# Kernel optimization log

Measured on AMD Instinct MI355X. Metric: run time of the kernel, lower is better.

The kernel has to match this reference:

```python
import jax, jax.numpy as jnp
import numpy as np

DIM = 768
NUM_HEADS = 12
HEAD_DIM = DIM // NUM_HEADS
HW = 32  # input_size = (32, 32)


def setup_inputs() -> dict:
    key = jax.random.key(0)
    ks = jax.random.split(key, 7)
    return {
        "x": jax.random.normal(ks[0], (8, HW, HW, DIM), dtype=jnp.float32),
        "w_qkv": jax.random.normal(ks[1], (DIM, 3 * DIM), dtype=jnp.float32) * 0.02,
        "b_qkv": jnp.zeros((3 * DIM,), dtype=jnp.float32),
        "w_proj": jax.random.normal(ks[2], (DIM, DIM), dtype=jnp.float32) * 0.02,
        "b_proj": jnp.zeros((DIM,), dtype=jnp.float32),
        "rel_pos_h": jax.random.normal(ks[3], (2 * HW - 1, HEAD_DIM), dtype=jnp.float32) * 0.02,
        "rel_pos_w": jax.random.normal(ks[4], (2 * HW - 1, HEAD_DIM), dtype=jnp.float32) * 0.02,
    }


def _gather_rel_pos(size, rel_pos):
    # q_size == k_size == size, so no resize; index = i - j + (size - 1)
    idx = jnp.arange(size)[:, None] - jnp.arange(size)[None, :] + (size - 1)
    return rel_pos[idx]  # [size, size, head_dim]


def reference(x, w_qkv, b_qkv, w_proj, b_proj, rel_pos_h, rel_pos_w):
    B, H, W, C = x.shape
    nH, D = NUM_HEADS, HEAD_DIM
    scale = D ** -0.5
    S = H * W

    qkv = x.reshape(B, S, C) @ w_qkv + b_qkv          # [B,S,3C]
    qkv = qkv.reshape(B, S, 3, nH, D).transpose(2, 0, 3, 1, 4)  # [3,B,nH,S,D]
    q, k, v = qkv[0], qkv[1], qkv[2]

    attn = jnp.einsum('bnsd,bntd->bnst', q * scale, k)  # [B,nH,S,S]

    # decomposed relative positional bias
    Rh = _gather_rel_pos(H, rel_pos_h)                  # [H,H,D]
    Rw = _gather_rel_pos(W, rel_pos_w)                  # [W,W,D]
    r_q = q.reshape(B, nH, H, W, D)
    rel_h = jnp.einsum('bnhwc,hkc->bnhwk', r_q, Rh)     # [B,nH,H,W,H]
    rel_w = jnp.einsum('bnhwc,wkc->bnhwk', r_q, Rw)     # [B,nH,H,W,W]
    attn = (attn.reshape(B, nH, H, W, H, W)
            + rel_h[..., :, None]
            + rel_w[..., None, :]).reshape(B, nH, S, S)

    attn = jax.nn.softmax(attn, axis=-1)
    out = jnp.einsum('bnst,bntd->bnsd', attn, v)        # [B,nH,S,D]
    out = out.transpose(0, 2, 1, 3).reshape(B, H, W, C)
    return out @ w_proj + b_proj
```

## Files before the change

### kernel.cpp

```cpp
#include <hip/hip_runtime.h>
#include <cstdint>
#include <cstddef>

#define NH 12
#define HDIM 64
#define C_ 768
#define C3 2304
#define SEQ 1024
#define LS 72
#define LSV 76
#define SMAX 6.0f
#define LOG2E 1.4426950408889634f

typedef short bf16x8_t __attribute__((ext_vector_type(8)));
typedef float f32x4_t __attribute__((ext_vector_type(4)));
typedef unsigned short u16x4_t __attribute__((ext_vector_type(4)));

__device__ __forceinline__ unsigned short bf16_rne(float x) {
    unsigned int u = __float_as_uint(x);
    u += 0x7FFFu + ((u >> 16) & 1u);
    return (unsigned short)(u >> 16);
}
__device__ __forceinline__ float bf16f(unsigned short h) {
    return __uint_as_float(((unsigned int)h) << 16);
}

__device__ __forceinline__ void load_lds16(const unsigned short* g, unsigned short* l) {
    auto gp = (const __attribute__((address_space(1))) unsigned short*)(uintptr_t)g;
    auto lp = (__attribute__((address_space(3))) unsigned short*)(uint32_t)(uintptr_t)l;
    __builtin_amdgcn_global_load_lds(gp, lp, 16, 0, 0);
}

__device__ __forceinline__ int swz(int row, int g) {
    const int pr = row >> 1;
    const int ch = (((row & 1) << 2) | g) ^ (pr & 7);
    return pr * 64 + ch * 8;
}

__device__ __forceinline__ void splitT_body(const float* __restrict__ W,
                                            unsigned short* __restrict__ Thi,
                                            unsigned short* __restrict__ Tlo,
                                            int Kdim, int Ndim, int kb, int nb,
                                            float (*tile)[33], int t)
{
    const int lr = t >> 3, lc = (t & 7) * 4;
    *(float4*)&tile[lr][lc] = *(const float4*)&W[(size_t)(kb + lr) * Ndim + nb + lc];
    __syncthreads();
    const float v0 = tile[lc + 0][lr];
    const float v1 = tile[lc + 1][lr];
    const float v2 = tile[lc + 2][lr];
    const float v3 = tile[lc + 3][lr];
    u16x4_t h, l;
    h.x = bf16_rne(v0); l.x = bf16_rne(v0 - bf16f(h.x));
    h.y = bf16_rne(v1); l.y = bf16_rne(v1 - bf16f(h.y));
    h.z = bf16_rne(v2); l.z = bf16_rne(v2 - bf16f(h.z));
    h.w = bf16_rne(v3); l.w = bf16_rne(v3 - bf16f(h.w));
    *(u16x4_t*)&Thi[(size_t)(nb + lr) * Kdim + kb + lc] = h;
    *(u16x4_t*)&Tlo[(size_t)(nb + lr) * Kdim + kb + lc] = l;
}

__global__ __launch_bounds__(256)
void prep_kernel(const float* __restrict__ x, const float* __restrict__ w_qkv,
                 const float* __restrict__ w_proj,
                 const float* __restrict__ rel_h, const float* __restrict__ rel_w,
                 unsigned short* __restrict__ xhi,
                 unsigned short* __restrict__ wqh, unsigned short* __restrict__ wql,
                 unsigned short* __restrict__ wph, unsigned short* __restrict__ wpl,
                 unsigned short* __restrict__ relcat)
{
    __shared__ float tile[32][33];
    const int bid = blockIdx.x, tid = threadIdx.x;
    if (bid < 6144) {
        const int i = bid * 256 + tid;
        float4 v = ((const float4*)x)[i];
        u16x4_t h;
        h.x = bf16_rne(v.x); h.y = bf16_rne(v.y); h.z = bf16_rne(v.z); h.w = bf16_rne(v.w);
        ((u16x4_t*)xhi)[i] = h;
    } else if (bid < 7872) {
        const int local = bid - 6144;
        const int bx = local % 72, by = local / 72;
        splitT_body(w_qkv, wqh, wql, C_, C3, by * 32, bx * 32, tile, tid);
    } else if (bid < 8448) {
        const int local = bid - 7872;
        const int bx = local % 24, by = local / 24;
        splitT_body(w_proj, wph, wpl, C_, C_, by * 32, bx * 32, tile, tid);
    } else {
        const int i = (bid - 8448) * 256 + tid;
        if (i < 2016) {
            const int j = i * 4;
            const int row = j >> 6, col = j & 63;
            const float* src = row < 63 ? &rel_h[row * 64 + col] : &rel_w[(row - 63) * 64 + col];
            const float4 v = *(const float4*)src;
            u16x4_t h;
            h.x = bf16_rne(v.x); h.y = bf16_rne(v.y); h.z = bf16_rne(v.z); h.w = bf16_rne(v.w);
            *(u16x4_t*)&relcat[j] = h;
        }
    }
}

__global__ __launch_bounds__(256, 4)
void qkvgemm_kernel(const unsigned short* __restrict__ Ahi, const unsigned short* __restrict__ BThi,
                    const float* __restrict__ bias,
                    unsigned short* __restrict__ q_hi, unsigned short* __restrict__ k_hi,
                    unsigned short* __restrict__ v_hi)
{
    constexpr int K = 768;
    __shared__ unsigned short As[2][4096];
    __shared__ unsigned short Bs[2][4096];
    const int tid = threadIdx.x;
    const int w = tid >> 6, lane = tid & 63, g = lane >> 4, r = lane & 15;
    const int wr = (w >> 1) * 64, wc = (w & 1) * 64;

    const int bid  = blockIdx.x;
    const int xcd  = bid & 7;
    const int idx  = bid >> 3;
    const int msub = idx & 7;
    const int ntile = idx >> 3;
    const int m0 = (xcd * 8 + msub) * 128;
    const int n0 = ntile * 128;

    int row_[2], gc_[2];
#pragma unroll
    for (int i = 0; i < 2; ++i) {
        const int s = i * 256 + tid;
        const int pr = s >> 3;
        const int u = (s & 7) ^ (pr & 7);
        row_[i] = pr * 2 + (u >> 2);
        gc_[i]  = u & 3;
    }
    const unsigned short* gA0 = Ahi + (size_t)(m0 + row_[0]) * K + gc_[0] * 8;
    const unsigned short* gA1 = Ahi + (size_t)(m0 + row_[1]) * K + gc_[1] * 8;
    const unsigned short* gB0 = BThi + (size_t)(n0 + row_[0]) * K + gc_[0] * 8;
    const unsigned short* gB1 = BThi + (size_t)(n0 + row_[1]) * K + gc_[1] * 8;
    const int lofs0 = w * 512;
    const int lofs1 = 2048 + w * 512;

    f32x4_t acc[4][4];
#pragma unroll
    for (int i = 0; i < 4; ++i)
#pragma unroll
        for (int j = 0; j < 4; ++j)
#pragma unroll
            for (int q = 0; q < 4; ++q) acc[i][j][q] = 0.f;

    load_lds16(gA0, &As[0][lofs0]);
    load_lds16(gA1, &As[0][lofs1]);
    load_lds16(gB0, &Bs[0][lofs0]);
    load_lds16(gB1, &Bs[0][lofs1]);

    int cur = 0;
    for (int k0 = 0; k0 < K; k0 += 32) {
        __syncthreads();
        if (k0 + 32 < K) {
            const int nb2 = cur ^ 1;
            load_lds16(gA0 + k0 + 32, &As[nb2][lofs0]);
            load_lds16(gA1 + k0 + 32, &As[nb2][lofs1]);
            load_lds16(gB0 + k0 + 32, &Bs[nb2][lofs0]);
            load_lds16(gB1 + k0 + 32, &Bs[nb2][lofs1]);
        }
        bf16x8_t am[4];
#pragma unroll
        for (int i = 0; i < 4; ++i)
            am[i] = *(const bf16x8_t*)&As[cur][swz(wr + 16 * i + r, g)];
        __builtin_amdgcn_s_setprio(1);
#pragma unroll
        for (int j = 0; j < 4; ++j) {
            const bf16x8_t bn = *(const bf16x8_t*)&Bs[cur][swz(wc + 16 * j + r, g)];
#pragma unroll
            for (int i = 0; i < 4; ++i)
                acc[i][j] = __builtin_amdgcn_mfma_f32_16x16x32_bf16(am[i], bn, acc[i][j], 0, 0, 0);
        }
        __builtin_amdgcn_s_setprio(0);
        cur ^= 1;
    }

    const int third = n0 >= 1536 ? 2 : (n0 >= 768 ? 1 : 0);
    unsigned short* outH = third == 2 ? v_hi : third == 1 ? k_hi : q_hi;
#pragma unroll
    for (int j = 0; j < 4; ++j) {
        const int n = n0 + wc + 16 * j + r;
        const float bj = bias[n];
        const int nn = n - third * 768;
        const int h = nn >> 6, d = nn & 63;
#pragma unroll
        for (int i = 0; i < 4; ++i) {
            const int m = m0 + wr + 16 * i + 4 * g;
            const int b = m >> 10, t = m & 1023;
            const size_t hb = ((size_t)(b * NH + h)) << 16;
            unsigned short* dh = outH + hb + (size_t)t * 64 + d;
#pragma unroll
            for (int q = 0; q < 4; ++q)
                dh[(size_t)q * 64] = bf16_rne(acc[i][j][q] + bj);
        }
    }
}

__global__ __launch_bounds__(256, 2)
void projgemm_kernel(const unsigned short* __restrict__ Ahi, const unsigned short* __restrict__ Alo,
                     const unsigned short* __restrict__ BThi, const unsigned short* __restrict__ BTlo,
                     const float* __restrict__ bias, float* __restrict__ C)
{
    constexpr int K = 768;
    constexpr int N = C_;
    __shared__ unsigned short Ash[2][4096], Asl[2][4096];
    __shared__ unsigned short Bsh[2][4096], Bsl[2][4096];
    const int tid = threadIdx.x;
    const int w = tid >> 6, lane = tid & 63, g = lane >> 4, r = lane & 15;
    const int wr = (w >> 1) * 64, wc = (w & 1) * 64;

    const int bid  = blockIdx.x;
    const int xcd  = bid & 7;
    const int idx  = bid >> 3;
    const int msub = idx & 7;
    const int ntile = idx >> 3;
    const int m0 = (xcd * 8 + msub) * 128;
    const int n0 = ntile * 128;

    int row_[2], gc_[2];
#pragma unroll
    for (int i = 0; i < 2; ++i) {
        const int s = i * 256 + tid;
        const int pr = s >> 3;
        const int u = (s & 7) ^ (pr & 7);
        row_[i] = pr * 2 + (u >> 2);
        gc_[i]  = u & 3;
    }
    const unsigned short* gAh0 = Ahi + (size_t)(m0 + row_[0]) * K + gc_[0] * 8;
    const unsigned short* gAh1 = Ahi + (size_t)(m0 + row_[1]) * K + gc_[1] * 8;
    const unsigned short* gAl0 = Alo + (size_t)(m0 + row_[0]) * K + gc_[0] * 8;
    const unsigned short* gAl1 = Alo + (size_t)(m0 + row_[1]) * K + gc_[1] * 8;
    const unsigned short* gBh0 = BThi + (size_t)(n0 + row_[0]) * K + gc_[0] * 8;
    const unsigned short* gBh1 = BThi + (size_t)(n0 + row_[1]) * K + gc_[1] * 8;
    const unsigned short* gBl0 = BTlo + (size_t)(n0 + row_[0]) * K + gc_[0] * 8;
    const unsigned short* gBl1 = BTlo + (size_t)(n0 + row_[1]) * K + gc_[1] * 8;
    const int lofs0 = w * 512;
    const int lofs1 = 2048 + w * 512;

    f32x4_t acc[4][4];
#pragma unroll
    for (int i = 0; i < 4; ++i)
#pragma unroll
        for (int j = 0; j < 4; ++j)
#pragma unroll
            for (int q = 0; q < 4; ++q) acc[i][j][q] = 0.f;

    load_lds16(gAh0, &Ash[0][lofs0]);
    load_lds16(gAh1, &Ash[0][lofs1]);
    load_lds16(gAl0, &Asl[0][lofs0]);
    load_lds16(gAl1, &Asl[0][lofs1]);
    load_lds16(gBh0, &Bsh[0][lofs0]);
    load_lds16(gBh1, &Bsh[0][lofs1]);
    load_lds16(gBl0, &Bsl[0][lofs0]);
    load_lds16(gBl1, &Bsl[0][lofs1]);

    int cur = 0;
    for (int k0 = 0; k0 < K; k0 += 32) {
        __syncthreads();
        if (k0 + 32 < K) {
            const int nb2 = cur ^ 1;
            load_lds16(gAh0 + k0 + 32, &Ash[nb2][lofs0]);
            load_lds16(gAh1 + k0 + 32, &Ash[nb2][lofs1]);
            load_lds16(gAl0 + k0 + 32, &Asl[nb2][lofs0]);
            load_lds16(gAl1 + k0 + 32, &Asl[nb2][lofs1]);
            load_lds16(gBh0 + k0 + 32, &Bsh[nb2][lofs0]);
            load_lds16(gBh1 + k0 + 32, &Bsh[nb2][lofs1]);
            load_lds16(gBl0 + k0 + 32, &Bsl[nb2][lofs0]);
            load_lds16(gBl1 + k0 + 32, &Bsl[nb2][lofs1]);
        }
        bf16x8_t amh[4], aml[4];
#pragma unroll
        for (int i = 0; i < 4; ++i) {
            const int o = swz(wr + 16 * i + r, g);
            amh[i] = *(const bf16x8_t*)&Ash[cur][o];
            aml[i] = *(const bf16x8_t*)&Asl[cur][o];
        }
        __builtin_amdgcn_s_setprio(1);
#pragma unroll
        for (int j = 0; j < 4; ++j) {
            const int o = swz(wc + 16 * j + r, g);
            const bf16x8_t bnh = *(const bf16x8_t*)&Bsh[cur][o];
            const bf16x8_t bnl = *(const bf16x8_t*)&Bsl[cur][o];
#pragma unroll
            for (int i = 0; i < 4; ++i) {
                acc[i][j] = __builtin_amdgcn_mfma_f32_16x16x32_bf16(amh[i], bnh, acc[i][j], 0, 0, 0);
                acc[i][j] = __builtin_amdgcn_mfma_f32_16x16x32_bf16(amh[i], bnl, acc[i][j], 0, 0, 0);
                acc[i][j] = __builtin_amdgcn_mfma_f32_16x16x32_bf16(aml[i], bnh, acc[i][j], 0, 0, 0);
            }
        }
        __builtin_amdgcn_s_setprio(0);
        cur ^= 1;
    }

#pragma unroll
    for (int j = 0; j < 4; ++j) {
        const float bj = bias[n0 + wc + 16 * j + r];
#pragma unroll
        for (int i = 0; i < 4; ++i) {
            float* Cp = C + (size_t)(m0 + wr + 16 * i + 4 * g) * N + n0 + wc + 16 * j + r;
#pragma unroll
            for (int q = 0; q < 4; ++q)
                Cp[(size_t)q * N] = acc[i][j][q] + bj;
        }
    }
}

__global__ __launch_bounds__(256, 4)
void relgemm_kernel(const unsigned short* __restrict__ qhi, const unsigned short* __restrict__ relcat,
                    unsigned short* __restrict__ G)
{
    __shared__ unsigned short bs[128 * LS];
    const int tid = threadIdx.x;
    const int sb = blockIdx.x, bh = blockIdx.y;
    const int w = tid >> 6, lane = tid & 63, g = lane >> 4, r = lane & 15;
    const size_t hb = (size_t)bh << 16;

    {
        const int row = tid >> 1, c32 = (tid & 1) * 32;
        if (row < 126) {
#pragma unroll
            for (int e = 0; e < 4; ++e)
                *(bf16x8_t*)&bs[row * LS + c32 + 8 * e] =
                    *(const bf16x8_t*)&relcat[row * 64 + c32 + 8 * e];
        } else {
            const bf16x8_t z = {0,0,0,0,0,0,0,0};
#pragma unroll
            for (int e = 0; e < 4; ++e)
                *(bf16x8_t*)&bs[row * LS + c32 + 8 * e] = z;
        }
    }
    bf16x8_t aq[2][2];
#pragma unroll
    for (int i = 0; i < 2; ++i)
#pragma unroll
        for (int c = 0; c < 2; ++c)
            aq[i][c] = *(const bf16x8_t*)(qhi + hb + (size_t)(sb * 128 + w * 32 + 16 * i + r) * 64 + c * 32 + 8 * g);
    __syncthreads();

    f32x4_t acc[2][8];
#pragma unroll
    for (int i = 0; i < 2; ++i)
#pragma unroll
        for (int fj = 0; fj < 8; ++fj)
#pragma unroll
            for (int q = 0; q < 4; ++q) acc[i][fj][q] = 0.f;

#pragma unroll
    for (int c = 0; c < 2; ++c)
#pragma unroll
        for (int fj = 0; fj < 8; ++fj) {
            const bf16x8_t brel = *(const bf16x8_t*)&bs[(16 * fj + r) * LS + c * 32 + 8 * g];
#pragma unroll
            for (int i = 0; i < 2; ++i)
                acc[i][fj] = __builtin_amdgcn_mfma_f32_16x16x32_bf16(aq[i][c], brel, acc[i][fj], 0, 0, 0);
        }

    unsigned short* Gb = G + (((size_t)bh << 10) + sb * 128 + w * 32) * 128;
#pragma unroll
    for (int i = 0; i < 2; ++i)
#pragma unroll
        for (int reg = 0; reg < 4; ++reg) {
            unsigned short* Gr = Gb + (size_t)(16 * i + 4 * g + reg) * 128 + r;
#pragma unroll
            for (int fj = 0; fj < 8; ++fj)
                Gr[16 * fj] = bf16_rne(acc[i][fj][reg]);
        }
}

__global__ __launch_bounds__(256, 4)
void attn11_kernel(const unsigned short* __restrict__ qhi,
                   const unsigned short* __restrict__ khi,
                   const unsigned short* __restrict__ vhi,
                   const unsigned short* __restrict__ G,
                   unsigned short* __restrict__ outh, unsigned short* __restrict__ outl)
{
    __shared__ unsigned short ksh[2 * 64 * LS];
    __shared__ unsigned short vsh[2 * 64 * LSV];

    const int tid  = threadIdx.x;
    const int bh   = blockIdx.x;
    const int s0   = blockIdx.y * 64;
    const int w    = tid >> 6;
    const int lane = tid & 63;
    const int g    = lane >> 4;
    const int r    = lane & 15;
    const size_t hb = (size_t)bh << 16;

    bf16x8_t aq[2];
#pragma unroll
    for (int c = 0; c < 2; ++c)
        aq[c] = *(const bf16x8_t*)(qhi + hb + (size_t)(s0 + w * 16 + r) * 64 + c * 32 + 8 * g);

    const unsigned short* Gbh = G + ((size_t)bh << 17);
    const int q    = s0 + w * 16 + r;
    const int qoff = q * 128;
    const int qcb  = (q >> 5) + 31;
    const int iw   = q & 31;
    float bw[4][2];
#pragma unroll
    for (int reg = 0; reg < 4; ++reg)
#pragma unroll
        for (int jh = 0; jh < 2; ++jh)
            bw[reg][jh] = bf16f(Gbh[qoff + 94 + iw - 16 * jh - 4 * g - reg]) * LOG2E;

    f32x4_t oacc[4];
    float lsum[4];
#pragma unroll
    for (int i = 0; i < 4; ++i) {
        lsum[i] = 0.f;
#pragma unroll
        for (int j = 0; j < 4; ++j) oacc[i][j] = 0.f;
    }

    const int krow = tid >> 2, kc16 = (tid & 3) * 16;
    const int tb = (tid >> 4) * 4, d0 = (tid & 15) * 4;
    const int addr_a = (((g & 1) << 5) + r) << 2;
    const int addr_b = addr_a + 64;
    const bool lowg = g < 2;

    {
        const unsigned short* kh = khi + hb + (size_t)krow * 64 + kc16;
        const bf16x8_t a0 = *(const bf16x8_t*)kh;
        const bf16x8_t a1 = *(const bf16x8_t*)(kh + 8);
        u16x4_t rv[4];
#pragma unroll
        for (int i = 0; i < 4; ++i)
            rv[i] = *(const u16x4_t*)(vhi + hb + (size_t)(tb + i) * 64 + d0);
        *(bf16x8_t*)&ksh[krow * LS + kc16]     = a0;
        *(bf16x8_t*)&ksh[krow * LS + kc16 + 8] = a1;
#pragma unroll
        for (int c2 = 0; c2 < 4; ++c2) {
            u16x4_t th;
            th.x = rv[0][c2]; th.y = rv[1][c2]; th.z = rv[2][c2]; th.w = rv[3][c2];
            *(u16x4_t*)&vsh[(d0 + c2) * LSV + tb] = th;
        }
    }
    __syncthreads();

    int cur = 0;
    for (int t0 = 0; t0 < SEQ; t0 += 64) {
        const int cok = cur * 64 * LS;
        const int cov = cur * 64 * LSV;
        const int tn = (t0 + 64 < SEQ) ? t0 + 64 : t0;
        bf16x8_t nk0, nk1;
        u16x4_t nv[4];
        {
            const unsigned short* kh = khi + hb + (size_t)(tn + krow) * 64 + kc16;
            nk0 = *(const bf16x8_t*)kh;
            nk1 = *(const bf16x8_t*)(kh + 8);
#pragma unroll
            for (int i = 0; i < 4; ++i)
                nv[i] = *(const u16x4_t*)(vhi + hb + (size_t)(tn + tb + i) * 64 + d0);
        }

        f32x4_t sacc[4];
#pragma unroll
        for (int fj = 0; fj < 4; ++fj)
#pragma unroll
            for (int j = 0; j < 4; ++j) sacc[fj][j] = 0.f;
        __builtin_amdgcn_s_setprio(1);
#pragma unroll
        for (int c = 0; c < 2; ++c)
#pragma unroll
            for (int fj = 0; fj < 4; ++fj) {
                const bf16x8_t bkh = *(const bf16x8_t*)&ksh[cok + (16 * fj + r) * LS + c * 32 + 8 * g];
                sacc[fj] = __builtin_amdgcn_mfma_f32_16x16x32_bf16(bkh, aq[c], sacc[fj], 0, 0, 0);
            }
        __builtin_amdgcn_s_setprio(0);

        const int kh0 = t0 >> 5;
        const float bh0 = (bf16f(Gbh[qoff + qcb - kh0])     - SMAX) * LOG2E;
        const float bh1 = (bf16f(Gbh[qoff + qcb - kh0 - 1]) - SMAX) * LOG2E;
#pragma unroll
        for (int fj = 0; fj < 4; ++fj)
#pragma unroll
            for (int reg = 0; reg < 4; ++reg) {
                const float s = fmaf(sacc[fj][reg], 0.125f * LOG2E,
                                     ((fj >> 1) ? bh1 : bh0) + bw[reg][fj & 1]);
                const float e = exp2f(s);
                sacc[fj][reg] = e;
                lsum[reg] += e;
            }

        unsigned int pk01[4], pk23[4];
#pragma unroll
        for (int fj = 0; fj < 4; ++fj) {
            asm("v_cvt_pk_bf16_f32 %0, %1, %2" : "=v"(pk01[fj]) : "v"(sacc[fj][0]), "v"(sacc[fj][1]));
            asm("v_cvt_pk_bf16_f32 %0, %1, %2" : "=v"(pk23[fj]) : "v"(sacc[fj][2]), "v"(sacc[fj][3]));
        }

#pragma unroll
        for (int c = 0; c < 2; ++c) {
            const int a01A = __builtin_amdgcn_ds_bpermute(addr_a, (int)pk01[2 * c]);
            const int a23A = __builtin_amdgcn_ds_bpermute(addr_a, (int)pk23[2 * c]);
            const int b01A = __builtin_amdgcn_ds_bpermute(addr_b, (int)pk01[2 * c]);
            const int b23A = __builtin_amdgcn_ds_bpermute(addr_b, (int)pk23[2 * c]);
            const int a01B = __builtin_amdgcn_ds_bpermute(addr_a, (int)pk01[2 * c + 1]);
            const int a23B = __builtin_amdgcn_ds_bpermute(addr_a, (int)pk23[2 * c + 1]);
            const int b01B = __builtin_amdgcn_ds_bpermute(addr_b, (int)pk01[2 * c + 1]);
            const int b23B = __builtin_amdgcn_ds_bpermute(addr_b, (int)pk23[2 * c + 1]);
            union { int u[4]; bf16x8_t v; } pf;
            pf.u[0] = lowg ? a01A : a01B;
            pf.u[1] = lowg ? a23A : a23B;
            pf.u[2] = lowg ? b01A : b01B;
            pf.u[3] = lowg ? b23A : b23B;
            __builtin_amdgcn_s_setprio(1);
#pragma unroll
            for (int fd = 0; fd < 4; ++fd) {
                const bf16x8_t bvh = *(const bf16x8_t*)&vsh[cov + (16 * fd + r) * LSV + c * 32 + 8 * g];
                oacc[fd] = __builtin_amdgcn_mfma_f32_16x16x32_bf16(bvh, pf.v, oacc[fd], 0, 0, 0);
            }
            __builtin_amdgcn_s_setprio(0);
        }

        const int nok = (cur ^ 1) * 64 * LS;
        const int nov = (cur ^ 1) * 64 * LSV;
        *(bf16x8_t*)&ksh[nok + krow * LS + kc16]     = nk0;
        *(bf16x8_t*)&ksh[nok + krow * LS + kc16 + 8] = nk1;
#pragma unroll
        for (int c2 = 0; c2 < 4; ++c2) {
            u16x4_t th;
            th.x = nv[0][c2]; th.y = nv[1][c2]; th.z = nv[2][c2]; th.w = nv[3][c2];
            *(u16x4_t*)&vsh[nov + (d0 + c2) * LSV + tb] = th;
        }
        __syncthreads();
        cur ^= 1;
    }

    const int b = bh / NH, h = bh - (bh / NH) * NH;
    float rs = (lsum[0] + lsum[1]) + (lsum[2] + lsum[3]);
    rs += __shfl_xor(rs, 16);
    rs += __shfl_xor(rs, 32);
    const float rinv = 1.f / rs;
    unsigned short* oph = outh + ((size_t)b * SEQ + q) * C_ + h * HDIM + 4 * g;
    unsigned short* opl = outl + ((size_t)b * SEQ + q) * C_ + h * HDIM + 4 * g;
#pragma unroll
    for (int fd = 0; fd < 4; ++fd) {
        u16x4_t hv, lv;
#pragma unroll
        for (int reg = 0; reg < 4; ++reg) {
            const float v = oacc[fd][reg] * rinv;
            const unsigned short hh = bf16_rne(v);
            hv[reg] = hh;
            lv[reg] = bf16_rne(v - bf16f(hh));
        }
        *(u16x4_t*)(oph + 16 * fd) = hv;
        *(u16x4_t*)(opl + 16 * fd) = lv;
    }
}

extern "C" void kernel_launch(void* const* d_in, const int* in_sizes, int n_in,
                              void* d_out, int out_size, void* d_ws, size_t ws_size,
                              hipStream_t stream) {
    (void)in_sizes; (void)n_in; (void)out_size; (void)ws_size;
    const float* x      = (const float*)d_in[0];
    const float* w_qkv  = (const float*)d_in[1];
    const float* b_qkv  = (const float*)d_in[2];
    const float* w_proj = (const float*)d_in[3];
    const float* b_proj = (const float*)d_in[4];
    const float* rel_h  = (const float*)d_in[5];
    const float* rel_w  = (const float*)d_in[6];
    float* out = (float*)d_out;

    char* base = (char*)d_ws;
    unsigned short* xhi    = (unsigned short*)(base + 0);
    unsigned short* xlo    = (unsigned short*)(base + 12582912);
    unsigned short* wqh    = (unsigned short*)(base + 25165824);
    unsigned short* wql    = (unsigned short*)(base + 28704768);
    unsigned short* wph    = (unsigned short*)(base + 32243712);
    unsigned short* wpl    = (unsigned short*)(base + 33423360);
    unsigned short* qhi    = (unsigned short*)(base + 34603008);
    unsigned short* relcat = (unsigned short*)(base + 47185920);
    unsigned short* khi    = (unsigned short*)(base + 59768832);
    unsigned short* vhi    = (unsigned short*)(base + 84934656);
    unsigned short* G      = (unsigned short*)(base + 110100480);
    unsigned short* ohif   = xhi;
    unsigned short* olo    = xlo;

    prep_kernel<<<8456, 256, 0, stream>>>(x, w_qkv, w_proj, rel_h, rel_w,
                                          xhi, wqh, wql, wph, wpl, relcat);
    qkvgemm_kernel<<<1152, 256, 0, stream>>>(xhi, wqh, b_qkv, qhi, khi, vhi);
    {
        dim3 grid(8, 96);
        relgemm_kernel<<<grid, 256, 0, stream>>>(qhi, relcat, G);
    }
    {
        dim3 grid(96, SEQ / 64);
        attn11_kernel<<<grid, 256, 0, stream>>>(qhi, khi, vhi, G, ohif, olo);
    }
    projgemm_kernel<<<384, 256, 0, stream>>>(ohif, olo, wph, wpl, b_proj, out);
}
```

Baseline: 166.8 us.

## Store V transposed from QKV GEMM epilogue and load it directly in attention

The QKV GEMM epilogue now writes V in a per-head [d][t] transposed layout, using 4-wide vector stores along t. The attention kernel can then copy V tiles into shared memory with two 16-byte loads and stores per thread, instead of gathering 4-element pieces and transposing them in registers. The change also drops the s_setprio hints around the MFMA loops in attention. This removes transpose work and narrow global loads from the attention inner loop, at the cost of a differently shaped store pattern in the GEMM epilogue.

```diff
diff --git a/kernel.cpp b/kernel.cpp
--- a/kernel.cpp
+++ b/kernel.cpp
@@ -102,7 +102,7 @@
 void qkvgemm_kernel(const unsigned short* __restrict__ Ahi, const unsigned short* __restrict__ BThi,
                     const float* __restrict__ bias,
                     unsigned short* __restrict__ q_hi, unsigned short* __restrict__ k_hi,
-                    unsigned short* __restrict__ v_hi)
+                    unsigned short* __restrict__ vT)
 {
     constexpr int K = 768;
     __shared__ unsigned short As[2][4096];
@@ -175,22 +175,43 @@
     }
 
     const int third = n0 >= 1536 ? 2 : (n0 >= 768 ? 1 : 0);
-    unsigned short* outH = third == 2 ? v_hi : third == 1 ? k_hi : q_hi;
-#pragma unroll
-    for (int j = 0; j < 4; ++j) {
-        const int n = n0 + wc + 16 * j + r;
-        const float bj = bias[n];
-        const int nn = n - third * 768;
-        const int h = nn >> 6, d = nn & 63;
-#pragma unroll
-        for (int i = 0; i < 4; ++i) {
-            const int m = m0 + wr + 16 * i + 4 * g;
-            const int b = m >> 10, t = m & 1023;
-            const size_t hb = ((size_t)(b * NH + h)) << 16;
-            unsigned short* dh = outH + hb + (size_t)t * 64 + d;
-#pragma unroll
-            for (int q = 0; q < 4; ++q)
-                dh[(size_t)q * 64] = bf16_rne(acc[i][j][q] + bj);
+    if (third == 2) {
+#pragma unroll
+        for (int j = 0; j < 4; ++j) {
+            const int n = n0 + wc + 16 * j + r;
+            const float bj = bias[n];
+            const int nn = n - 1536;
+            const int h = nn >> 6, d = nn & 63;
+#pragma unroll
+            for (int i = 0; i < 4; ++i) {
+                const int m = m0 + wr + 16 * i + 4 * g;
+                const int b = m >> 10, t = m & 1023;
+                const size_t hb = ((size_t)(b * NH + h)) << 16;
+                u16x4_t pv;
+#pragma unroll
+                for (int q = 0; q < 4; ++q)
+                    pv[q] = bf16_rne(acc[i][j][q] + bj);
+                *(u16x4_t*)&vT[hb + (size_t)d * 1024 + t] = pv;
+            }
+        }
+    } else {
+        unsigned short* outH = third == 1 ? k_hi : q_hi;
+#pragma unroll
+        for (int j = 0; j < 4; ++j) {
+            const int n = n0 + wc + 16 * j + r;
+            const float bj = bias[n];
+            const int nn = n - third * 768;
+            const int h = nn >> 6, d = nn & 63;
+#pragma unroll
+            for (int i = 0; i < 4; ++i) {
+                const int m = m0 + wr + 16 * i + 4 * g;
+                const int b = m >> 10, t = m & 1023;
+                const size_t hb = ((size_t)(b * NH + h)) << 16;
+                unsigned short* dh = outH + hb + (size_t)t * 64 + d;
+#pragma unroll
+                for (int q = 0; q < 4; ++q)
+                    dh[(size_t)q * 64] = bf16_rne(acc[i][j][q] + bj);
+            }
         }
     }
 }
@@ -367,9 +388,9 @@
 }
 
 __global__ __launch_bounds__(256, 4)
-void attn11_kernel(const unsigned short* __restrict__ qhi,
+void attn12_kernel(const unsigned short* __restrict__ qhi,
                    const unsigned short* __restrict__ khi,
-                   const unsigned short* __restrict__ vhi,
+                   const unsigned short* __restrict__ vT,
                    const unsigned short* __restrict__ G,
                    unsigned short* __restrict__ outh, unsigned short* __restrict__ outl)
 {
@@ -412,7 +433,7 @@
     }
 
     const int krow = tid >> 2, kc16 = (tid & 3) * 16;
-    const int tb = (tid >> 4) * 4, d0 = (tid & 15) * 4;
+    const int vd = tid >> 3, vt = (tid & 7) * 8;
     const int addr_a = (((g & 1) << 5) + r) << 2;
     const int addr_b = addr_a + 64;
     const bool lowg = g < 2;
@@ -421,18 +442,12 @@
         const unsigned short* kh = khi + hb + (size_t)krow * 64 + kc16;
         const bf16x8_t a0 = *(const bf16x8_t*)kh;
         const bf16x8_t a1 = *(const bf16x8_t*)(kh + 8);
-        u16x4_t rv[4];
-#pragma unroll
-        for (int i = 0; i < 4; ++i)
-            rv[i] = *(const u16x4_t*)(vhi + hb + (size_t)(tb + i) * 64 + d0);
+        const bf16x8_t va = *(const bf16x8_t*)(vT + hb + (size_t)vd * 1024 + vt);
+        const bf16x8_t vb = *(const bf16x8_t*)(vT + hb + (size_t)(vd + 32) * 1024 + vt);
         *(bf16x8_t*)&ksh[krow * LS + kc16]     = a0;
         *(bf16x8_t*)&ksh[krow * LS + kc16 + 8] = a1;
-#pragma unroll
-        for (int c2 = 0; c2 < 4; ++c2) {
-            u16x4_t th;
-            th.x = rv[0][c2]; th.y = rv[1][c2]; th.z = rv[2][c2]; th.w = rv[3][c2];
-            *(u16x4_t*)&vsh[(d0 + c2) * LSV + tb] = th;
-        }
+        *(bf16x8_t*)&vsh[vd * LSV + vt]        = va;
+        *(bf16x8_t*)&vsh[(vd + 32) * LSV + vt] = vb;
     }
     __syncthreads();
 
@@ -441,15 +456,13 @@
         const int cok = cur * 64 * LS;
         const int cov = cur * 64 * LSV;
         const int tn = (t0 + 64 < SEQ) ? t0 + 64 : t0;
-        bf16x8_t nk0, nk1;
-        u16x4_t nv[4];
+        bf16x8_t nk0, nk1, nva, nvb;
         {
             const unsigned short* kh = khi + hb + (size_t)(tn + krow) * 64 + kc16;
             nk0 = *(const bf16x8_t*)kh;
             nk1 = *(const bf16x8_t*)(kh + 8);
-#pragma unroll
-            for (int i = 0; i < 4; ++i)
-                nv[i] = *(const u16x4_t*)(vhi + hb + (size_t)(tn + tb + i) * 64 + d0);
+            nva = *(const bf16x8_t*)(vT + hb + (size_t)vd * 1024 + tn + vt);
+            nvb = *(const bf16x8_t*)(vT + hb + (size_t)(vd + 32) * 1024 + tn + vt);
         }
 
         f32x4_t sacc[4];
@@ -457,7 +470,6 @@
         for (int fj = 0; fj < 4; ++fj)
 #pragma unroll
             for (int j = 0; j < 4; ++j) sacc[fj][j] = 0.f;
-        __builtin_amdgcn_s_setprio(1);
 #pragma unroll
         for (int c = 0; c < 2; ++c)
 #pragma unroll
@@ -465,7 +477,6 @@
                 const bf16x8_t bkh = *(const bf16x8_t*)&ksh[cok + (16 * fj + r) * LS + c * 32 + 8 * g];
                 sacc[fj] = __builtin_amdgcn_mfma_f32_16x16x32_bf16(bkh, aq[c], sacc[fj], 0, 0, 0);
             }
-        __builtin_amdgcn_s_setprio(0);
 
         const int kh0 = t0 >> 5;
         const float bh0 = (bf16f(Gbh[qoff + qcb - kh0])     - SMAX) * LOG2E;
@@ -503,25 +514,19 @@
             pf.u[1] = lowg ? a23A : a23B;
             pf.u[2] = lowg ? b01A : b01B;
             pf.u[3] = lowg ? b23A : b23B;
-            __builtin_amdgcn_s_setprio(1);
 #pragma unroll
             for (int fd = 0; fd < 4; ++fd) {
                 const bf16x8_t bvh = *(const bf16x8_t*)&vsh[cov + (16 * fd + r) * LSV + c * 32 + 8 * g];
                 oacc[fd] = __builtin_amdgcn_mfma_f32_16x16x32_bf16(bvh, pf.v, oacc[fd], 0, 0, 0);
             }
-            __builtin_amdgcn_s_setprio(0);
         }
 
         const int nok = (cur ^ 1) * 64 * LS;
         const int nov = (cur ^ 1) * 64 * LSV;
-        *(bf16x8_t*)&ksh[nok + krow * LS + kc16]     = nk0;
-        *(bf16x8_t*)&ksh[nok + krow * LS + kc16 + 8] = nk1;
-#pragma unroll
-        for (int c2 = 0; c2 < 4; ++c2) {
-            u16x4_t th;
-            th.x = nv[0][c2]; th.y = nv[1][c2]; th.z = nv[2][c2]; th.w = nv[3][c2];
-            *(u16x4_t*)&vsh[nov + (d0 + c2) * LSV + tb] = th;
-        }
+        *(bf16x8_t*)&ksh[nok + krow * LS + kc16]      = nk0;
+        *(bf16x8_t*)&ksh[nok + krow * LS + kc16 + 8]  = nk1;
+        *(bf16x8_t*)&vsh[nov + vd * LSV + vt]         = nva;
+        *(bf16x8_t*)&vsh[nov + (vd + 32) * LSV + vt]  = nvb;
         __syncthreads();
         cur ^= 1;
     }
@@ -571,21 +576,21 @@
     unsigned short* qhi    = (unsigned short*)(base + 34603008);
     unsigned short* relcat = (unsigned short*)(base + 47185920);
     unsigned short* khi    = (unsigned short*)(base + 59768832);
-    unsigned short* vhi    = (unsigned short*)(base + 84934656);
+    unsigned short* vT     = (unsigned short*)(base + 84934656);
     unsigned short* G      = (unsigned short*)(base + 110100480);
     unsigned short* ohif   = xhi;
     unsigned short* olo    = xlo;
 
     prep_kernel<<<8456, 256, 0, stream>>>(x, w_qkv, w_proj, rel_h, rel_w,
                                           xhi, wqh, wql, wph, wpl, relcat);
-    qkvgemm_kernel<<<1152, 256, 0, stream>>>(xhi, wqh, b_qkv, qhi, khi, vhi);
+    qkvgemm_kernel<<<1152, 256, 0, stream>>>(xhi, wqh, b_qkv, qhi, khi, vT);
     {
         dim3 grid(8, 96);
         relgemm_kernel<<<grid, 256, 0, stream>>>(qhi, relcat, G);
     }
     {
         dim3 grid(96, SEQ / 64);
-        attn11_kernel<<<grid, 256, 0, stream>>>(qhi, khi, vhi, G, ohif, olo);
+        attn12_kernel<<<grid, 256, 0, stream>>>(qhi, khi, vT, G, ohif, olo);
     }
     projgemm_kernel<<<384, 256, 0, stream>>>(ohif, olo, wph, wpl, b_proj, out);
 }
```

Result: faster. 162.2 us (median of 3 runs) (-2.8%).
